# Kernel optimization log

Measured on AMD Instinct MI355X. Metric: run time of the kernel, lower is better.

## Reference

```python
import jax, jax.numpy as jnp
import numpy as np

N_NODES = 100000
N_EDGES = 1600000
D_IN = 64
D_OUT = 64


def setup_inputs() -> dict:
    key = jax.random.key(0)
    k1, k2, k3, k4, k5 = jax.random.split(key, 5)
    x = jax.random.normal(k1, (N_NODES, D_IN), dtype=jnp.float32)
    edge_index = jax.random.randint(k2, (2, N_EDGES), 0, N_NODES, dtype=jnp.int64)
    dist_vec = jax.random.uniform(k3, (N_EDGES,), dtype=jnp.float32)
    # Linear params (xavier-uniform-like scale for W)
    limit = float(np.sqrt(6.0 / (D_IN + D_OUT)))
    W = jax.random.uniform(k4, (D_OUT, D_IN), minval=-limit, maxval=limit, dtype=jnp.float32)
    b = jax.random.uniform(k5, (D_OUT,), minval=-limit, maxval=limit, dtype=jnp.float32)
    return {"x": x, "edge_index": edge_index, "dist_vec": dist_vec, "W": W, "b": b}


def reference(x, edge_index, dist_vec, W, b):
    row, col = edge_index[0], edge_index[1]
    n = x.shape[0]
    # degree of destination (col) nodes
    deg = jax.ops.segment_sum(jnp.ones_like(dist_vec), col, num_segments=n)
    deg_inv_sqrt = jnp.where(deg > 0, jax.lax.rsqrt(deg), 0.0)
    norm = deg_inv_sqrt[row] * deg_inv_sqrt[col]  # [E]
    w = jnp.exp(-dist_vec ** 2) * norm            # [E]
    # sparse.mm(adj, x): out[row] += w * x[col]
    msgs = w[:, None] * x[col]                    # [E, D_IN]
    side_embed = jax.ops.segment_sum(msgs, row, num_segments=n)  # [N, D_IN]
    return side_embed @ W.T + b
```

## Files before the change

### kernel.cpp

```cpp
#include <hip/hip_runtime.h>
#include <hip/hip_fp16.h>


constexpr int NN   = 100000;
constexpr int NE   = 1600000;
constexpr int D    = 64;
constexpr int NRB  = (NN + 63) / 64;
constexpr int NCB  = (NN + 255) / 256;
constexpr int HB   = 250;
constexpr int HT   = 1024;
constexpr int PT   = 512;
constexpr int YGB  = 512;
constexpr int GT   = 512;
constexpr int CHUNK = NE / HB;
constexpr int NSR  = NRB * HB;
constexpr int NSCC = NCB * HB;
constexpr int NST  = NSR + NSCC;
constexpr int SCB  = 1024;
constexpr int SCG  = (NST + SCB - 1) / SCB;
constexpr int CAP  = 1536;

using f16x8 = __attribute__((ext_vector_type(8))) _Float16;
using f32x4 = __attribute__((ext_vector_type(4))) float;

__global__ void __launch_bounds__(PT)
prep_kernel(const float* __restrict__ x, const float* __restrict__ W,
            __half* __restrict__ y, const int* __restrict__ row,
            const int* __restrict__ col, int* __restrict__ hist) {
    __shared__ int hr[NRB], hc[NCB];
    const int t = threadIdx.x;
    const int blk = blockIdx.x;
    if (blk < HB) {
        for (int i = t; i < NRB; i += PT) hr[i] = 0;
        for (int i = t; i < NCB; i += PT) hc[i] = 0;
        __syncthreads();
        const int e0 = blk * CHUNK;
        for (int e = e0 + t * 4; e < e0 + CHUNK; e += PT * 4) {
            const int4 r4 = *reinterpret_cast<const int4*>(row + e);
            const int4 c4 = *reinterpret_cast<const int4*>(col + e);
            atomicAdd(&hr[r4.x >> 6], 1); atomicAdd(&hr[r4.y >> 6], 1);
            atomicAdd(&hr[r4.z >> 6], 1); atomicAdd(&hr[r4.w >> 6], 1);
            atomicAdd(&hc[c4.x >> 8], 1); atomicAdd(&hc[c4.y >> 8], 1);
            atomicAdd(&hc[c4.z >> 8], 1); atomicAdd(&hc[c4.w >> 8], 1);
        }
        __syncthreads();
        for (int i = t; i < NRB; i += PT) hist[i * HB + blk] = hr[i];
        for (int i = t; i < NCB; i += PT) hist[NSR + i * HB + blk] = hc[i];
    } else {
        const int m  = t & 15;
        const int kb = (t & 63) >> 4;
        f16x8 bf[4][2];
        #pragma unroll
        for (int jt = 0; jt < 4; ++jt) {
            #pragma unroll
            for (int kh = 0; kh < 2; ++kh) {
                const float* wp = W + (size_t)(jt * 16 + m) * 64 + kh * 32 + kb * 8;
                const float4 w0 = *reinterpret_cast<const float4*>(wp);
                const float4 w1 = *reinterpret_cast<const float4*>(wp + 4);
                f16x8 f;
                f[0] = (_Float16)w0.x; f[1] = (_Float16)w0.y;
                f[2] = (_Float16)w0.z; f[3] = (_Float16)w0.w;
                f[4] = (_Float16)w1.x; f[5] = (_Float16)w1.y;
                f[6] = (_Float16)w1.z; f[7] = (_Float16)w1.w;
                bf[jt][kh] = f;
            }
        }
        const int wid = ((blk - HB) * PT + t) >> 6;
        const int nw  = (YGB * PT) >> 6;
        for (int nt = wid; nt < NN / 16; nt += nw) {
            const int n0 = nt * 16;
            f16x8 af[2];
            #pragma unroll
            for (int kh = 0; kh < 2; ++kh) {
                const float* xp = x + (size_t)(n0 + m) * 64 + kh * 32 + kb * 8;
                const float4 x0 = *reinterpret_cast<const float4*>(xp);
                const float4 x1 = *reinterpret_cast<const float4*>(xp + 4);
                f16x8 f;
                f[0] = (_Float16)x0.x; f[1] = (_Float16)x0.y;
                f[2] = (_Float16)x0.z; f[3] = (_Float16)x0.w;
                f[4] = (_Float16)x1.x; f[5] = (_Float16)x1.y;
                f[6] = (_Float16)x1.z; f[7] = (_Float16)x1.w;
                af[kh] = f;
            }
            #pragma unroll
            for (int jt = 0; jt < 4; ++jt) {
                f32x4 acc = {0.f, 0.f, 0.f, 0.f};
                acc = __builtin_amdgcn_mfma_f32_16x16x32_f16(bf[jt][0], af[0], acc, 0, 0, 0);
                acc = __builtin_amdgcn_mfma_f32_16x16x32_f16(bf[jt][1], af[1], acc, 0, 0, 0);
                const size_t elem = (size_t)(n0 + m) * 64 + jt * 16 + kb * 4;
                union { uint2 u; __half h[4]; } pk;
                pk.h[0] = __float2half(acc[0]); pk.h[1] = __float2half(acc[1]);
                pk.h[2] = __float2half(acc[2]); pk.h[3] = __float2half(acc[3]);
                *reinterpret_cast<uint2*>(y + elem) = pk.u;
            }
        }
    }
}

__global__ void scanpart_kernel(const int* __restrict__ a, int* __restrict__ bsum) {
    __shared__ int red[16];
    const int t = threadIdx.x;
    const int i = blockIdx.x * SCB + t;
    int s = (i < NST) ? a[i] : 0;
    #pragma unroll
    for (int o = 1; o < 64; o <<= 1) s += __shfl_xor(s, o);
    if ((t & 63) == 0) red[t >> 6] = s;
    __syncthreads();
    if (t < 16) {
        int ss = red[t];
        #pragma unroll
        for (int o = 1; o < 16; o <<= 1) ss += __shfl_xor(ss, o);
        if (t == 0) bsum[blockIdx.x] = ss;
    }
}

__global__ void scanfinal_kernel(int* __restrict__ a, const int* __restrict__ bsum) {
    __shared__ int wsum[16], wsum2[16], red[16];
    __shared__ int prefix_s;
    const int t = threadIdx.x;
    const int i = blockIdx.x * SCB + t;
    const int lane = t & 63;
    const int w = t >> 6;
    int pv = (t < blockIdx.x) ? bsum[t] : 0;
    #pragma unroll
    for (int o = 1; o < 64; o <<= 1) pv += __shfl_xor(pv, o);
    if (lane == 0) red[w] = pv;
    const int v = (i < NST) ? a[i] : 0;
    int s = v;
    #pragma unroll
    for (int o = 1; o < 64; o <<= 1) { int u = __shfl_up(s, o); if (lane >= o) s += u; }
    if (lane == 63) wsum[w] = s;
    __syncthreads();
    if (t < 16) {
        int ss = wsum[t];
        #pragma unroll
        for (int o = 1; o < 16; o <<= 1) { int u = __shfl_up(ss, o); if (t >= o) ss += u; }
        wsum2[t] = ss;
        int rr = red[t];
        #pragma unroll
        for (int o = 1; o < 16; o <<= 1) rr += __shfl_xor(rr, o);
        if (t == 0) prefix_s = rr;
    }
    __syncthreads();
    const int excl = prefix_s + (w ? wsum2[w - 1] : 0) + (s - v);
    if (i < NST) a[i] = excl;
}

__global__ void __launch_bounds__(HT)
scatboth_kernel(const int* __restrict__ row, const int* __restrict__ col,
                const float* __restrict__ dist, const int* __restrict__ hoff,
                unsigned* __restrict__ payload, unsigned char* __restrict__ colidx) {
    __shared__ int cur_r[NRB];
    __shared__ int cur_c[NCB];
    const int t = threadIdx.x;
    for (int i = t; i < NRB; i += HT) cur_r[i] = hoff[i * HB + blockIdx.x];
    for (int i = t; i < NCB; i += HT) cur_c[i] = hoff[NSR + i * HB + blockIdx.x] - NE;
    __syncthreads();
    const int e0 = blockIdx.x * CHUNK;
    for (int e = e0 + t * 4; e < e0 + CHUNK; e += HT * 4) {
        const int4 r4 = *reinterpret_cast<const int4*>(row + e);
        const int4 c4 = *reinterpret_cast<const int4*>(col + e);
        const float4 d4 = *reinterpret_cast<const float4*>(dist + e);
        const int rr[4] = {r4.x, r4.y, r4.z, r4.w};
        const int cc[4] = {c4.x, c4.y, c4.z, c4.w};
        const float dd[4] = {d4.x, d4.y, d4.z, d4.w};
        #pragma unroll
        for (int j = 0; j < 4; ++j) {
            const int r = rr[j];
            const int c = cc[j];
            const float dv = dd[j];
            const unsigned w8 = (unsigned)(__expf(-dv * dv) * 255.0f + 0.5f);
            const int pr = atomicAdd(&cur_r[r >> 6], 1);
            payload[pr] = ((unsigned)(r & 63) << 25) | (w8 << 17) | (unsigned)c;
            const int pc = atomicAdd(&cur_c[c >> 8], 1);
            colidx[pc] = (unsigned char)(c & 255);
        }
    }
}

__global__ void __launch_bounds__(256)
coldinv_kernel(const int* __restrict__ hoff, const unsigned char* __restrict__ colidx,
               float* __restrict__ dinv) {
    __shared__ int cnt[256];
    const int t = threadIdx.x;
    const int b = blockIdx.x;
    cnt[t] = 0;
    __syncthreads();
    const int s0 = hoff[NSR + b * HB] - NE;
    const int s1 = (b + 1 < NCB) ? (hoff[NSR + (b + 1) * HB] - NE) : NE;
    for (int k = s0 + t; k < s1; k += 256) atomicAdd(&cnt[colidx[k]], 1);
    __syncthreads();
    const int n = b * 256 + t;
    if (n < NN) {
        const int d = cnt[t];
        dinv[n] = (d > 0) ? rsqrtf((float)d) : 0.0f;
    }
}

__global__ void __launch_bounds__(GT)
gather_fused_kernel(const int* __restrict__ hoff, const unsigned* __restrict__ payload,
                    const float* __restrict__ dinvg, const __half* __restrict__ y,
                    const float* __restrict__ bias, float* __restrict__ out) {
    __shared__ unsigned stage[CAP];
    __shared__ unsigned sorted[CAP];
    __shared__ int cnt[64], cur[64], rs[65];
    __shared__ float dinv_s[64];
    const int t = threadIdx.x;
    const int lane = t & 63;
    const int wv = t >> 6;
    const int b = blockIdx.x;
    const int sub = lane >> 3;
    const int ch8 = (lane & 7) << 3;
    constexpr float WSCL = 1.0f / 255.0f;
    const float4 b0 = *reinterpret_cast<const float4*>(bias + ch8);
    const float4 b1 = *reinterpret_cast<const float4*>(bias + ch8 + 4);

    if (t < 64) {
        cnt[t] = 0;
        const int n = b * 64 + t;
        dinv_s[t] = (n < NN) ? dinvg[n] : 0.0f;
    }
    const int s0g = hoff[b * HB];
    const int s1g = (b + 1 < NRB) ? hoff[(b + 1) * HB] : NE;
    int ne = s1g - s0g;
    ne = (ne < CAP) ? ne : CAP;
    __syncthreads();
    for (int k = t; k < ne; k += GT) {
        const unsigned p = payload[s0g + k];
        stage[k] = p;
        atomicAdd(&cnt[p >> 25], 1);
    }
    __syncthreads();
    if (t < 64) {
        const int v = cnt[t];
        int s = v;
        #pragma unroll
        for (int o = 1; o < 64; o <<= 1) { int u = __shfl_up(s, o); if (t >= o) s += u; }
        cur[t] = s - v;
        rs[t] = s - v;
        if (t == 63) rs[64] = s;
    }
    __syncthreads();
    for (int k = t; k < ne; k += GT) {
        const unsigned p = stage[k];
        const int pos = atomicAdd(&cur[p >> 25], 1);
        sorted[pos] = p;
    }
    __syncthreads();

    for (int ln = wv; ln < 64; ln += 8) {
        const int n = b * 64 + ln;
        if (n >= NN) break;
        const int e0 = rs[ln];
        const int e1 = rs[ln + 1];
        float a0 = 0.f, a1 = 0.f, a2 = 0.f, a3 = 0.f;
        float a4 = 0.f, a5 = 0.f, a6 = 0.f, a7 = 0.f;
        for (int p0 = e0; p0 < e1; p0 += 8) {
            const int pp = p0 + sub;
            const int ppc = (pp < e1) ? pp : (e1 - 1);
            const unsigned m = sorted[ppc];
            const int c = (int)(m & 0x1FFFFu);
            float wgt = (float)((m >> 17) & 255u) * WSCL * dinvg[c];
            wgt = (pp < e1) ? wgt : 0.0f;
            const float4 raw = *reinterpret_cast<const float4*>(y + (size_t)c * 64 + ch8);
            const __half2* h2 = reinterpret_cast<const __half2*>(&raw);
            const float2 f0 = __half22float2(h2[0]);
            const float2 f1 = __half22float2(h2[1]);
            const float2 f2 = __half22float2(h2[2]);
            const float2 f3 = __half22float2(h2[3]);
            a0 += wgt * f0.x; a1 += wgt * f0.y; a2 += wgt * f1.x; a3 += wgt * f1.y;
            a4 += wgt * f2.x; a5 += wgt * f2.y; a6 += wgt * f3.x; a7 += wgt * f3.y;
        }
        #pragma unroll
        for (int o = 8; o < 64; o <<= 1) {
            a0 += __shfl_xor(a0, o); a1 += __shfl_xor(a1, o);
            a2 += __shfl_xor(a2, o); a3 += __shfl_xor(a3, o);
            a4 += __shfl_xor(a4, o); a5 += __shfl_xor(a5, o);
            a6 += __shfl_xor(a6, o); a7 += __shfl_xor(a7, o);
        }
        if (sub == 0) {
            const float dn = dinv_s[ln];
            const float4 o0 = make_float4(b0.x + dn * a0, b0.y + dn * a1,
                                          b0.z + dn * a2, b0.w + dn * a3);
            const float4 o1 = make_float4(b1.x + dn * a4, b1.y + dn * a5,
                                          b1.z + dn * a6, b1.w + dn * a7);
            float* op = out + (size_t)n * 64 + ch8;
            *reinterpret_cast<float4*>(op)     = o0;
            *reinterpret_cast<float4*>(op + 4) = o1;
        }
    }
}

extern "C" void kernel_launch(void* const* d_in, const int* in_sizes, int n_in,
                              void* d_out, int out_size, void* d_ws, size_t ws_size,
                              hipStream_t stream) {
    const float* x    = (const float*)d_in[0];
    const int*   ei   = (const int*)d_in[1];
    const float* dist = (const float*)d_in[2];
    const float* W    = (const float*)d_in[3];
    const float* b    = (const float*)d_in[4];
    float* out = (float*)d_out;

    const int* row = ei;
    const int* col = ei + NE;

    unsigned*      payload = (unsigned*)d_ws;
    __half*        y       = (__half*)(payload + NE);
    int*           hist    = (int*)(y + (size_t)NN * 64);
    int*           bsum    = hist + NST;
    unsigned char* colidx  = (unsigned char*)(bsum + SCG);
    float*         dinv    = (float*)(colidx + NE);

    prep_kernel     <<<HB + YGB, PT, 0, stream>>>(x, W, y, row, col, hist);
    scanpart_kernel <<<SCG, SCB, 0, stream>>>(hist, bsum);
    scanfinal_kernel<<<SCG, SCB, 0, stream>>>(hist, bsum);
    scatboth_kernel <<<HB, HT, 0, stream>>>(row, col, dist, hist, payload, colidx);
    coldinv_kernel  <<<NCB, 256, 0, stream>>>(hist, colidx, dinv);
    gather_fused_kernel<<<NRB, GT, 0, stream>>>(hist, payload, dinv, y, b, out);
}
```

Baseline: 112.0 us.

## Split row/col scatter into separate blocks and gather two nodes per wave

The scatter kernel now launches twice as many blocks: half scatter row payloads and half scatter column indices, so the two atomic streams run on separate blocks with smaller shared state. The gather loop processes two destination nodes per wavefront at once, with separate accumulators, to raise memory-level parallelism on the y loads. This costs more registers and wasted lanes when the two nodes differ in degree, and the col-part blocks reread col.

```diff
diff --git a/kernel.cpp b/kernel.cpp
--- a/kernel.cpp
+++ b/kernel.cpp
@@ -150,30 +150,42 @@
 scatboth_kernel(const int* __restrict__ row, const int* __restrict__ col,
                 const float* __restrict__ dist, const int* __restrict__ hoff,
                 unsigned* __restrict__ payload, unsigned char* __restrict__ colidx) {
-    __shared__ int cur_r[NRB];
-    __shared__ int cur_c[NCB];
-    const int t = threadIdx.x;
-    for (int i = t; i < NRB; i += HT) cur_r[i] = hoff[i * HB + blockIdx.x];
-    for (int i = t; i < NCB; i += HT) cur_c[i] = hoff[NSR + i * HB + blockIdx.x] - NE;
-    __syncthreads();
-    const int e0 = blockIdx.x * CHUNK;
-    for (int e = e0 + t * 4; e < e0 + CHUNK; e += HT * 4) {
-        const int4 r4 = *reinterpret_cast<const int4*>(row + e);
-        const int4 c4 = *reinterpret_cast<const int4*>(col + e);
-        const float4 d4 = *reinterpret_cast<const float4*>(dist + e);
-        const int rr[4] = {r4.x, r4.y, r4.z, r4.w};
-        const int cc[4] = {c4.x, c4.y, c4.z, c4.w};
-        const float dd[4] = {d4.x, d4.y, d4.z, d4.w};
-        #pragma unroll
-        for (int j = 0; j < 4; ++j) {
-            const int r = rr[j];
-            const int c = cc[j];
-            const float dv = dd[j];
-            const unsigned w8 = (unsigned)(__expf(-dv * dv) * 255.0f + 0.5f);
-            const int pr = atomicAdd(&cur_r[r >> 6], 1);
-            payload[pr] = ((unsigned)(r & 63) << 25) | (w8 << 17) | (unsigned)c;
-            const int pc = atomicAdd(&cur_c[c >> 8], 1);
-            colidx[pc] = (unsigned char)(c & 255);
+    __shared__ int cur[NRB];
+    const int t = threadIdx.x;
+    const bool rowpart = blockIdx.x < HB;
+    const int blk = rowpart ? blockIdx.x : (blockIdx.x - HB);
+    const int e0 = blk * CHUNK;
+    if (rowpart) {
+        for (int i = t; i < NRB; i += HT) cur[i] = hoff[i * HB + blk];
+        __syncthreads();
+        for (int e = e0 + t * 4; e < e0 + CHUNK; e += HT * 4) {
+            const int4 r4 = *reinterpret_cast<const int4*>(row + e);
+            const int4 c4 = *reinterpret_cast<const int4*>(col + e);
+            const float4 d4 = *reinterpret_cast<const float4*>(dist + e);
+            const int rr[4] = {r4.x, r4.y, r4.z, r4.w};
+            const int cc[4] = {c4.x, c4.y, c4.z, c4.w};
+            const float dd[4] = {d4.x, d4.y, d4.z, d4.w};
+            #pragma unroll
+            for (int j = 0; j < 4; ++j) {
+                const int r = rr[j];
+                const float dv = dd[j];
+                const unsigned w8 = (unsigned)(__expf(-dv * dv) * 255.0f + 0.5f);
+                const int pr = atomicAdd(&cur[r >> 6], 1);
+                payload[pr] = ((unsigned)(r & 63) << 25) | (w8 << 17) | (unsigned)cc[j];
+            }
+        }
+    } else {
+        for (int i = t; i < NCB; i += HT) cur[i] = hoff[NSR + i * HB + blk] - NE;
+        __syncthreads();
+        for (int e = e0 + t * 4; e < e0 + CHUNK; e += HT * 4) {
+            const int4 c4 = *reinterpret_cast<const int4*>(col + e);
+            const int cc[4] = {c4.x, c4.y, c4.z, c4.w};
+            #pragma unroll
+            for (int j = 0; j < 4; ++j) {
+                const int c = cc[j];
+                const int pc = atomicAdd(&cur[c >> 8], 1);
+                colidx[pc] = (unsigned char)(c & 255);
+            }
         }
     }
 }
@@ -248,28 +260,49 @@
     }
     __syncthreads();
 
-    for (int ln = wv; ln < 64; ln += 8) {
-        const int n = b * 64 + ln;
-        if (n >= NN) break;
-        const int e0 = rs[ln];
-        const int e1 = rs[ln + 1];
+    const int ne1 = (ne > 0) ? (ne - 1) : 0;
+    #pragma unroll
+    for (int pr = 0; pr < 4; ++pr) {
+        const int lnA = wv + pr * 16;
+        const int lnB = lnA + 8;
+        const int e0A = rs[lnA], e1A = rs[lnA + 1];
+        const int e0B = rs[lnB], e1B = rs[lnB + 1];
+        const int itA = (e1A - e0A + 7) >> 3;
+        const int itB = (e1B - e0B + 7) >> 3;
+        const int iters = (itA > itB) ? itA : itB;
         float a0 = 0.f, a1 = 0.f, a2 = 0.f, a3 = 0.f;
         float a4 = 0.f, a5 = 0.f, a6 = 0.f, a7 = 0.f;
-        for (int p0 = e0; p0 < e1; p0 += 8) {
-            const int pp = p0 + sub;
-            const int ppc = (pp < e1) ? pp : (e1 - 1);
-            const unsigned m = sorted[ppc];
-            const int c = (int)(m & 0x1FFFFu);
-            float wgt = (float)((m >> 17) & 255u) * WSCL * dinvg[c];
-            wgt = (pp < e1) ? wgt : 0.0f;
-            const float4 raw = *reinterpret_cast<const float4*>(y + (size_t)c * 64 + ch8);
-            const __half2* h2 = reinterpret_cast<const __half2*>(&raw);
-            const float2 f0 = __half22float2(h2[0]);
-            const float2 f1 = __half22float2(h2[1]);
-            const float2 f2 = __half22float2(h2[2]);
-            const float2 f3 = __half22float2(h2[3]);
-            a0 += wgt * f0.x; a1 += wgt * f0.y; a2 += wgt * f1.x; a3 += wgt * f1.y;
-            a4 += wgt * f2.x; a5 += wgt * f2.y; a6 += wgt * f3.x; a7 += wgt * f3.y;
+        float c0 = 0.f, c1 = 0.f, c2 = 0.f, c3 = 0.f;
+        float c4 = 0.f, c5 = 0.f, c6 = 0.f, c7 = 0.f;
+        for (int i = 0; i < iters; ++i) {
+            const int ppA = e0A + i * 8 + sub;
+            const int ppB = e0B + i * 8 + sub;
+            const bool okA = ppA < e1A;
+            const bool okB = ppB < e1B;
+            const unsigned mA = sorted[okA ? ppA : ne1];
+            const unsigned mB = sorted[okB ? ppB : ne1];
+            const int cA = (int)(mA & 0x1FFFFu);
+            const int cB = (int)(mB & 0x1FFFFu);
+            float wA = (float)((mA >> 17) & 255u) * WSCL * dinvg[cA];
+            float wB = (float)((mB >> 17) & 255u) * WSCL * dinvg[cB];
+            wA = okA ? wA : 0.0f;
+            wB = okB ? wB : 0.0f;
+            const float4 rawA = *reinterpret_cast<const float4*>(y + (size_t)cA * 64 + ch8);
+            const float4 rawB = *reinterpret_cast<const float4*>(y + (size_t)cB * 64 + ch8);
+            const __half2* hA = reinterpret_cast<const __half2*>(&rawA);
+            const __half2* hB = reinterpret_cast<const __half2*>(&rawB);
+            const float2 fA0 = __half22float2(hA[0]);
+            const float2 fA1 = __half22float2(hA[1]);
+            const float2 fA2 = __half22float2(hA[2]);
+            const float2 fA3 = __half22float2(hA[3]);
+            a0 += wA * fA0.x; a1 += wA * fA0.y; a2 += wA * fA1.x; a3 += wA * fA1.y;
+            a4 += wA * fA2.x; a5 += wA * fA2.y; a6 += wA * fA3.x; a7 += wA * fA3.y;
+            const float2 fB0 = __half22float2(hB[0]);
+            const float2 fB1 = __half22float2(hB[1]);
+            const float2 fB2 = __half22float2(hB[2]);
+            const float2 fB3 = __half22float2(hB[3]);
+            c0 += wB * fB0.x; c1 += wB * fB0.y; c2 += wB * fB1.x; c3 += wB * fB1.y;
+            c4 += wB * fB2.x; c5 += wB * fB2.y; c6 += wB * fB3.x; c7 += wB * fB3.y;
         }
         #pragma unroll
         for (int o = 8; o < 64; o <<= 1) {
@@ -277,14 +310,29 @@
             a2 += __shfl_xor(a2, o); a3 += __shfl_xor(a3, o);
             a4 += __shfl_xor(a4, o); a5 += __shfl_xor(a5, o);
             a6 += __shfl_xor(a6, o); a7 += __shfl_xor(a7, o);
-        }
-        if (sub == 0) {
-            const float dn = dinv_s[ln];
+            c0 += __shfl_xor(c0, o); c1 += __shfl_xor(c1, o);
+            c2 += __shfl_xor(c2, o); c3 += __shfl_xor(c3, o);
+            c4 += __shfl_xor(c4, o); c5 += __shfl_xor(c5, o);
+            c6 += __shfl_xor(c6, o); c7 += __shfl_xor(c7, o);
+        }
+        const int nA = b * 64 + lnA;
+        const int nB = b * 64 + lnB;
+        if (sub == 0 && nA < NN) {
+            const float dn = dinv_s[lnA];
             const float4 o0 = make_float4(b0.x + dn * a0, b0.y + dn * a1,
                                           b0.z + dn * a2, b0.w + dn * a3);
             const float4 o1 = make_float4(b1.x + dn * a4, b1.y + dn * a5,
                                           b1.z + dn * a6, b1.w + dn * a7);
-            float* op = out + (size_t)n * 64 + ch8;
+            float* op = out + (size_t)nA * 64 + ch8;
+            *reinterpret_cast<float4*>(op)     = o0;
+            *reinterpret_cast<float4*>(op + 4) = o1;
+        } else if (sub == 1 && nB < NN) {
+            const float dn = dinv_s[lnB];
+            const float4 o0 = make_float4(b0.x + dn * c0, b0.y + dn * c1,
+                                          b0.z + dn * c2, b0.w + dn * c3);
+            const float4 o1 = make_float4(b1.x + dn * c4, b1.y + dn * c5,
+                                          b1.z + dn * c6, b1.w + dn * c7);
+            float* op = out + (size_t)nB * 64 + ch8;
             *reinterpret_cast<float4*>(op)     = o0;
             *reinterpret_cast<float4*>(op + 4) = o1;
         }
@@ -314,7 +362,7 @@
     prep_kernel     <<<HB + YGB, PT, 0, stream>>>(x, W, y, row, col, hist);
     scanpart_kernel <<<SCG, SCB, 0, stream>>>(hist, bsum);
     scanfinal_kernel<<<SCG, SCB, 0, stream>>>(hist, bsum);
-    scatboth_kernel <<<HB, HT, 0, stream>>>(row, col, dist, hist, payload, colidx);
+    scatboth_kernel <<<HB * 2, HT, 0, stream>>>(row, col, dist, hist, payload, colidx);
     coldinv_kernel  <<<NCB, 256, 0, stream>>>(hist, colidx, dinv);
     gather_fused_kernel<<<NRB, GT, 0, stream>>>(hist, payload, dinv, y, b, out);
 }
```

After: 106.7 us, median of 2. 1.05x faster.
